# Kernel tuning notes

Hardware: AMD Instinct MI355X
Metric: run time of the kernel (lower is better)

The kernel has to match this reference:

```python
import jax, jax.numpy as jnp
import numpy as np

jax.config.update("jax_enable_x64", True)  # needed for faithful int64 topology hash (31**i weights)

B, SEQ, HID, OUT = 64, 2048, 1024, 1024
MAX_DEPTH = 3
MAX_NODES = 2 ** MAX_DEPTH - 1          # 7
MAX_LEAVES = 2 ** (MAX_DEPTH - 1)       # 4 leaf slots (nodes 3..6)
MAX_SHAPE_IDS = 256


def _gelu(x):
    return jax.nn.gelu(x, approximate=False)  # torch nn.GELU default = exact erf


def setup_inputs() -> dict:
    key = jax.random.key(0)
    ks = jax.random.split(key, 8)
    states = jax.random.normal(ks[0], (B, SEQ, HID), dtype=jnp.float32)

    rng = np.random.default_rng(0)
    lengths = rng.integers(SEQ // 2, SEQ, size=(B,)).astype(np.int64)
    # sorted segment boundaries within [0, lengths), first boundary at 0
    fr = np.sort(rng.random((B, MAX_LEAVES - 1)), axis=1)
    boundaries = np.concatenate(
        [np.zeros((B, 1), np.int64), np.floor(fr * lengths[:, None]).astype(np.int64)], axis=1)
    mask = np.arange(SEQ)[None, :] < lengths[:, None]
    # complete binary tree, depth 3: node 0 root, nodes 1-2 internal, 3-6 leaves
    leaf_order = np.tile(np.arange(MAX_NODES // 2, MAX_NODES, dtype=np.int64), (B, 1))
    active = np.ones((B, MAX_NODES), bool)
    is_leaf = np.concatenate([np.zeros((B, 3), bool), np.ones((B, 4), bool)], axis=1)
    left_child = np.array([1, 3, 5, -1, -1, -1, -1], np.int64)
    right_child = np.array([2, 4, 6, -1, -1, -1, -1], np.int64)
    depth = np.array([0, 1, 1, 2, 2, 2, 2], np.int64)

    def lin(k, fan_in, shape):
        return jax.random.normal(k, shape, dtype=jnp.float32) / np.sqrt(fan_in).astype(np.float32)

    W1 = lin(ks[1], HID, (HID, OUT)); b1 = jnp.zeros((OUT,), jnp.float32)
    W2 = lin(ks[2], OUT, (OUT, OUT)); b2 = jnp.zeros((OUT,), jnp.float32)
    Wm1 = lin(ks[3], 2 * OUT, (2 * OUT, OUT)); bm1 = jnp.zeros((OUT,), jnp.float32)
    Wm2 = lin(ks[4], OUT, (OUT, OUT)); bm2 = jnp.zeros((OUT,), jnp.float32)
    depth_embed = jax.random.normal(ks[5], (MAX_DEPTH, OUT), dtype=jnp.float32) * 0.02
    shape_embed = jax.random.normal(ks[6], (MAX_SHAPE_IDS, OUT), dtype=jnp.float32) * 0.02

    return dict(
        states=states, mask=jnp.asarray(mask), lengths=jnp.asarray(lengths),
        boundaries=jnp.asarray(boundaries), leaf_order=jnp.asarray(leaf_order),
        active=jnp.asarray(active), is_leaf=jnp.asarray(is_leaf),
        left_child=jnp.asarray(left_child), right_child=jnp.asarray(right_child),
        depth=jnp.asarray(depth),
        W1=W1, b1=b1, W2=W2, b2=b2, Wm1=Wm1, bm1=bm1, Wm2=Wm2, bm2=bm2,
        depth_embed=depth_embed, shape_embed=shape_embed)


def _forward(states, W1, b1, W2, b2, Wm1, bm1, Wm2, bm2, depth_embed, shape_embed,
             mask, lengths, boundaries, leaf_order, active, is_leaf,
             left_child, right_child, depth):
    b, seq, _ = states.shape
    S = boundaries.shape[1]
    max_nodes = left_child.shape[0]

    # ---- 1. vectorized ragged masked segment-mean pooling ----
    pos = jnp.arange(seq)
    # segment id per token: number of boundaries <= t, minus 1
    seg_id = (pos[None, None, :] >= boundaries[:, :, None]).sum(1) - 1      # (b, seq)
    valid = mask & (pos[None, :] < lengths[:, None]) & (seg_id >= 0)
    onehot = ((seg_id[:, :, None] == jnp.arange(S)[None, None, :])
              & valid[:, :, None]).astype(states.dtype)                     # (b, seq, S)
    cnt = onehot.sum(1)                                                     # (b, S)
    pooled = jnp.einsum('bts,bth->bsh', onehot, states) / jnp.clip(cnt, 1.0)[..., None]

    # ---- 2. encode segments + depth embedding, scatter to leaf slots ----
    enc = _gelu(pooled @ W1 + b1) @ W2 + b2                                 # (b, S, D)
    nidx = leaf_order                                                       # (b, S)
    nclip = jnp.maximum(nidx, 0)
    enc = enc + depth_embed[depth[nclip]]
    leaf_ok = (nidx >= 0) & jnp.take_along_axis(is_leaf, nclip, axis=1) & (cnt > 0)
    contrib = enc * leaf_ok[..., None].astype(enc.dtype)
    node_repr = jnp.zeros((b, max_nodes, enc.shape[-1]), enc.dtype)
    node_repr = node_repr.at[jnp.arange(b)[:, None], nclip].add(contrib)

    # ---- 3. bottom-up binary tree merge (loop over fixed small node count) ----
    for i in range(max_nodes - 1, -1, -1):
        lc = left_child[i]
        rc = right_child[i]
        is_int = active[:, i] & ~is_leaf[:, i]                              # (b,)
        l = jnp.take(node_repr, jnp.maximum(lc, 0), axis=1)                 # (b, D)
        r = jnp.take(node_repr, jnp.maximum(rc, 0), axis=1)
        merged = (_gelu(jnp.concatenate([l, r], axis=-1) @ Wm1 + bm1) @ Wm2 + bm2
                  + depth_embed[depth[i]])
        upd = is_int.any() & (lc != -1)
        newv = jnp.where(upd, merged * is_int[:, None].astype(merged.dtype),
                         node_repr[:, i])
        node_repr = node_repr.at[:, i].set(newv)

    # ---- 4. topology hash -> shape embedding ----
    pattern = active.astype(jnp.int64) * 2 + is_leaf.astype(jnp.int64)      # (b, nodes)
    weights = 31 ** jnp.arange(max_nodes, dtype=jnp.int64)
    hashed = (pattern * weights[None, :]).sum(1)
    shape_ids = jnp.abs(hashed) % shape_embed.shape[0]
    return node_repr[:, 0] + shape_embed[shape_ids]


def reference(states, mask, lengths, boundaries, leaf_order, active, is_leaf,
              left_child, right_child, depth,
              W1, b1, W2, b2, Wm1, bm1, Wm2, bm2, depth_embed, shape_embed):
    return _forward(states, W1, b1, W2, b2, Wm1, bm1, Wm2, bm2,
                    depth_embed, shape_embed, mask, lengths, boundaries,
                    leaf_order, active, is_leaf, left_child, right_child, depth)
```

## Files before the change

kernel.cpp:

```cpp
#include <hip/hip_runtime.h>
#include <cstdint>
#include <cstddef>

#define SEQ   2048
#define HID   1024
#define NBAT  64
#define NSEG  4
#define NNODE 7
#define TCHUNK 128

__device__ __forceinline__ float gelu_f(float x) {
  return 0.5f * x * (1.0f + erff(x * 0.7071067811865476f));
}

__global__ __launch_bounds__(256) void pool_kernel(
    const float* __restrict__ states, const int* __restrict__ boundaries,
    const int* __restrict__ lengths, float* __restrict__ pooled_sum)
{
  const int tc = blockIdx.x, b = blockIdx.y;
  const int tid = threadIdx.x;
  const int len = lengths[b];
  int bnd[5];
  bnd[0] = boundaries[b * 4 + 0];
  bnd[1] = boundaries[b * 4 + 1];
  bnd[2] = boundaries[b * 4 + 2];
  bnd[3] = boundaries[b * 4 + 3];
  bnd[4] = len;
  const int clo = tc * TCHUNK, chi = clo + TCHUNK;
  const float4* S = (const float4*)(states + (size_t)b * SEQ * HID);

  #pragma unroll
  for (int s = 0; s < NSEG; ++s) {
    int lo = bnd[s]     > clo ? bnd[s]     : clo;
    int hi = bnd[s + 1] < chi ? bnd[s + 1] : chi;
    if (lo >= hi) continue;
    float4 acc = make_float4(0.f, 0.f, 0.f, 0.f);
    int t = lo;
    for (; t + 4 <= hi; t += 4) {
      float4 v0 = S[(size_t)(t + 0) * (HID / 4) + tid];
      float4 v1 = S[(size_t)(t + 1) * (HID / 4) + tid];
      float4 v2 = S[(size_t)(t + 2) * (HID / 4) + tid];
      float4 v3 = S[(size_t)(t + 3) * (HID / 4) + tid];
      acc.x += (v0.x + v1.x) + (v2.x + v3.x);
      acc.y += (v0.y + v1.y) + (v2.y + v3.y);
      acc.z += (v0.z + v1.z) + (v2.z + v3.z);
      acc.w += (v0.w + v1.w) + (v2.w + v3.w);
    }
    for (; t < hi; ++t) {
      float4 v = S[(size_t)t * (HID / 4) + tid];
      acc.x += v.x; acc.y += v.y; acc.z += v.z; acc.w += v.w;
    }
    float* dst = pooled_sum + (size_t)(b * NSEG + s) * HID + tid * 4;
    atomicAdd(dst + 0, acc.x);
    atomicAdd(dst + 1, acc.y);
    atomicAdd(dst + 2, acc.z);
    atomicAdd(dst + 3, acc.w);
  }
}

#define BM 32
#define BN 64
#define BK 32

template<int AMODE, int EPI>
__global__ __launch_bounds__(256) void gemm_kernel(
    const float* __restrict__ A, const float* __restrict__ W,
    const float* __restrict__ bias, float* __restrict__ C,
    int M, int K,
    const int* __restrict__ boundaries, const int* __restrict__ lengths,
    const int* __restrict__ leaf_order, const int* __restrict__ active,
    const int* __restrict__ is_leaf, const int* __restrict__ depth,
    const int* __restrict__ left_child, const int* __restrict__ right_child,
    const float* __restrict__ dembed, const float* __restrict__ sembed,
    const float* __restrict__ node_in, float* __restrict__ node_out,
    int nodeA, int nodeB)
{
  const int N = 1024;
  __shared__ float As[BK][BM + 2];
  __shared__ float Ws[BK][BN];

  const int tid = threadIdx.x;
  const int n0 = blockIdx.x * BN;
  const int m0 = blockIdx.y * BM;

  const int am = tid >> 3;
  const int ak = (tid & 7) * 4;
  const int wk = tid >> 3;
  const int wn = (tid & 7) * 8;
  const int rm = (tid >> 4) * 2;
  const int cn = (tid & 15) * 4;

  float ainv = 1.0f;
  int lcn = 0, rcn = 0, arow_b = 0;
  if (AMODE == 1) {
    int m = m0 + am; int b = m >> 2; int s = m & 3;
    int bs = boundaries[b * 4 + s];
    int bn = (s < 3) ? boundaries[b * 4 + s + 1] : lengths[b];
    ainv = 1.0f / fmaxf((float)(bn - bs), 1.0f);
  } else if (AMODE == 2) {
    int mrow = m0 + am; int mi = mrow >> 6; int b = mrow & 63;
    int node = mi ? nodeB : nodeA;
    lcn = left_child[node]; rcn = right_child[node];
    arow_b = b;
  }

  float acc[2][4] = {{0.f,0.f,0.f,0.f},{0.f,0.f,0.f,0.f}};

  float4 av, wv0, wv1;
  {
    if (AMODE == 2) {
      int col = ak;
      int child = (col < 1024) ? lcn : rcn;
      av = *(const float4*)(node_in + (size_t)(arow_b * NNODE + child) * 1024 + (col & 1023));
    } else {
      av = *(const float4*)(A + (size_t)(m0 + am) * K + ak);
    }
    wv0 = *(const float4*)(W + (size_t)wk * N + n0 + wn);
    wv1 = *(const float4*)(W + (size_t)wk * N + n0 + wn + 4);
  }

  for (int k0 = 0; k0 < K; k0 += BK) {
    __syncthreads();
    As[ak + 0][am] = av.x * ainv;
    As[ak + 1][am] = av.y * ainv;
    As[ak + 2][am] = av.z * ainv;
    As[ak + 3][am] = av.w * ainv;
    *(float4*)&Ws[wk][wn]     = wv0;
    *(float4*)&Ws[wk][wn + 4] = wv1;
    __syncthreads();

    const int kn = k0 + BK;
    if (kn < K) {
      if (AMODE == 2) {
        int col = kn + ak;
        int child = (col < 1024) ? lcn : rcn;
        av = *(const float4*)(node_in + (size_t)(arow_b * NNODE + child) * 1024 + (col & 1023));
      } else {
        av = *(const float4*)(A + (size_t)(m0 + am) * K + kn + ak);
      }
      wv0 = *(const float4*)(W + (size_t)(kn + wk) * N + n0 + wn);
      wv1 = *(const float4*)(W + (size_t)(kn + wk) * N + n0 + wn + 4);
    }

    #pragma unroll
    for (int kk = 0; kk < BK; ++kk) {
      float2 a2 = *(const float2*)&As[kk][rm];
      float4 w  = *(const float4*)&Ws[kk][cn];
      acc[0][0] += a2.x * w.x; acc[0][1] += a2.x * w.y;
      acc[0][2] += a2.x * w.z; acc[0][3] += a2.x * w.w;
      acc[1][0] += a2.y * w.x; acc[1][1] += a2.y * w.y;
      acc[1][2] += a2.y * w.z; acc[1][3] += a2.y * w.w;
    }
  }

  #pragma unroll
  for (int r = 0; r < 2; ++r) {
    const int m = m0 + rm + r;
    const int n = n0 + cn;
    float4 x;
    x.x = acc[r][0] + bias[n + 0];
    x.y = acc[r][1] + bias[n + 1];
    x.z = acc[r][2] + bias[n + 2];
    x.w = acc[r][3] + bias[n + 3];

    if (EPI == 0) {
      x.x = gelu_f(x.x); x.y = gelu_f(x.y); x.z = gelu_f(x.z); x.w = gelu_f(x.w);
      *(float4*)(C + (size_t)m * N + n) = x;
    } else if (EPI == 1) {
      int b = m >> 2; int s = m & 3;
      int node  = leaf_order[b * 4 + s];
      int nclip = node < 0 ? 0 : node;
      int bs = boundaries[b * 4 + s];
      int bn = (s < 3) ? boundaries[b * 4 + s + 1] : lengths[b];
      bool ok = (node >= 0) && (is_leaf[b * NNODE + nclip] != 0) && (bn - bs > 0);
      int d = depth[nclip];
      const float* de = dembed + (size_t)d * 1024 + n;
      float sc = ok ? 1.0f : 0.0f;
      x.x = (x.x + de[0]) * sc; x.y = (x.y + de[1]) * sc;
      x.z = (x.z + de[2]) * sc; x.w = (x.w + de[3]) * sc;
      *(float4*)(node_out + (size_t)(b * NNODE + nclip) * 1024 + n) = x;
    } else if (EPI == 2) {
      int mi = m >> 6; int b = m & 63;
      int node = mi ? nodeB : nodeA;
      bool ii = (active[b * NNODE + node] != 0) && (is_leaf[b * NNODE + node] == 0);
      int d = depth[node];
      const float* de = dembed + (size_t)d * 1024 + n;
      float sc = ii ? 1.0f : 0.0f;
      x.x = (x.x + de[0]) * sc; x.y = (x.y + de[1]) * sc;
      x.z = (x.z + de[2]) * sc; x.w = (x.w + de[3]) * sc;
      *(float4*)(node_out + (size_t)(b * NNODE + node) * 1024 + n) = x;
    } else {
      int b = m & 63;
      bool ii = (active[b * NNODE + 0] != 0) && (is_leaf[b * NNODE + 0] == 0);
      int d = depth[0];
      const float* de = dembed + (size_t)d * 1024 + n;
      float sc = ii ? 1.0f : 0.0f;
      long long h = 0, w = 1;
      #pragma unroll
      for (int i = 0; i < NNODE; ++i) {
        long long p = (long long)active[b * NNODE + i] * 2
                    + (long long)is_leaf[b * NNODE + i];
        h += p * w;
        w *= 31;
      }
      long long a = h < 0 ? -h : h;
      int sid = (int)(a % 256);
      const float* se = sembed + (size_t)sid * 1024 + n;
      x.x = (x.x + de[0]) * sc + se[0];
      x.y = (x.y + de[1]) * sc + se[1];
      x.z = (x.z + de[2]) * sc + se[2];
      x.w = (x.w + de[3]) * sc + se[3];
      *(float4*)(node_out + (size_t)b * 1024 + n) = x;
    }
  }
}

extern "C" void kernel_launch(void* const* d_in, const int* in_sizes, int n_in,
                              void* d_out, int out_size, void* d_ws, size_t ws_size,
                              hipStream_t stream)
{
  const float* states     = (const float*)d_in[0];
  const int* lengths      = (const int*)d_in[2];
  const int* boundaries   = (const int*)d_in[3];
  const int* leaf_order   = (const int*)d_in[4];
  const int* active       = (const int*)d_in[5];
  const int* is_leaf      = (const int*)d_in[6];
  const int* left_child   = (const int*)d_in[7];
  const int* right_child  = (const int*)d_in[8];
  const int* depth        = (const int*)d_in[9];
  const float* W1  = (const float*)d_in[10];
  const float* b1  = (const float*)d_in[11];
  const float* W2  = (const float*)d_in[12];
  const float* b2  = (const float*)d_in[13];
  const float* Wm1 = (const float*)d_in[14];
  const float* bm1 = (const float*)d_in[15];
  const float* Wm2 = (const float*)d_in[16];
  const float* bm2 = (const float*)d_in[17];
  const float* dembed = (const float*)d_in[18];
  const float* sembed = (const float*)d_in[19];
  float* out = (float*)d_out;

  float* pooled    = (float*)d_ws;
  float* H1        = pooled + 256 * 1024;
  float* Hm        = H1 + 256 * 1024;
  float* node_repr = Hm + 128 * 1024;

  hipMemsetAsync(pooled, 0, (size_t)256 * 1024 * sizeof(float), stream);

  pool_kernel<<<dim3(SEQ / TCHUNK, NBAT), 256, 0, stream>>>(
      states, boundaries, lengths, pooled);

  gemm_kernel<1, 0><<<dim3(16, 8), 256, 0, stream>>>(
      pooled, W1, b1, H1, 256, 1024,
      boundaries, lengths, leaf_order, active, is_leaf, depth,
      left_child, right_child, dembed, sembed, nullptr, nullptr, -1, -1);

  gemm_kernel<0, 1><<<dim3(16, 8), 256, 0, stream>>>(
      H1, W2, b2, nullptr, 256, 1024,
      boundaries, lengths, leaf_order, active, is_leaf, depth,
      left_child, right_child, dembed, sembed, nullptr, node_repr, -1, -1);

  gemm_kernel<2, 0><<<dim3(16, 4), 256, 0, stream>>>(
      nullptr, Wm1, bm1, Hm, 128, 2048,
      boundaries, lengths, leaf_order, active, is_leaf, depth,
      left_child, right_child, dembed, sembed, node_repr, nullptr, 1, 2);
  gemm_kernel<0, 2><<<dim3(16, 4), 256, 0, stream>>>(
      Hm, Wm2, bm2, nullptr, 128, 1024,
      boundaries, lengths, leaf_order, active, is_leaf, depth,
      left_child, right_child, dembed, sembed, nullptr, node_repr, 1, 2);

  gemm_kernel<2, 0><<<dim3(16, 2), 256, 0, stream>>>(
      nullptr, Wm1, bm1, Hm, 64, 2048,
      boundaries, lengths, leaf_order, active, is_leaf, depth,
      left_child, right_child, dembed, sembed, node_repr, nullptr, 0, 0);
  gemm_kernel<0, 3><<<dim3(16, 2), 256, 0, stream>>>(
      Hm, Wm2, bm2, nullptr, 64, 1024,
      boundaries, lengths, leaf_order, active, is_leaf, depth,
      left_child, right_child, dembed, sembed, nullptr, out, 0, 0);
}
```

Baseline: 966.7 us.

## Split-K the tree GEMMs and fuse partial reduction with bias-GELU into A-loads

Each GEMM now splits K across blockIdx.z and writes partial sums to workspace. The following GEMM sums the partials, adds bias and applies GELU while loading its A tile. Separate small reduction kernels apply the bias and node epilogues. This raises block counts for the small-M tree GEMMs, which previously launched only 32-128 blocks, at the cost of extra partial-buffer traffic, redundant GELU recompute, and more launches.

New measurement: 812.2 us. 16.0% less time.

```diff
diff --git a/kernel.cpp b/kernel.cpp
--- a/kernel.cpp
+++ b/kernel.cpp
@@ -62,18 +62,16 @@
 #define BN 64
 #define BK 32
 
-template<int AMODE, int EPI>
+template<int AMODE, int SPLIT, int SRCS>
 __global__ __launch_bounds__(256) void gemm_kernel(
-    const float* __restrict__ A, const float* __restrict__ W,
-    const float* __restrict__ bias, float* __restrict__ C,
+    const float* __restrict__ A,
+    const float* __restrict__ W,
+    const float* __restrict__ biasA,
+    float* __restrict__ Cp,
     int M, int K,
     const int* __restrict__ boundaries, const int* __restrict__ lengths,
-    const int* __restrict__ leaf_order, const int* __restrict__ active,
-    const int* __restrict__ is_leaf, const int* __restrict__ depth,
     const int* __restrict__ left_child, const int* __restrict__ right_child,
-    const float* __restrict__ dembed, const float* __restrict__ sembed,
-    const float* __restrict__ node_in, float* __restrict__ node_out,
-    int nodeA, int nodeB)
+    const float* __restrict__ node_in, int nodeA, int nodeB)
 {
   const int N = 1024;
   __shared__ float As[BK][BM + 2];
@@ -82,6 +80,9 @@
   const int tid = threadIdx.x;
   const int n0 = blockIdx.x * BN;
   const int m0 = blockIdx.y * BM;
+  const int z  = blockIdx.z;
+  const int Kloc = K / SPLIT;
+  const int kbeg = z * Kloc;
 
   const int am = tid >> 3;
   const int ak = (tid & 7) * 4;
@@ -92,12 +93,12 @@
 
   float ainv = 1.0f;
   int lcn = 0, rcn = 0, arow_b = 0;
-  if (AMODE == 1) {
+  if constexpr (AMODE == 1) {
     int m = m0 + am; int b = m >> 2; int s = m & 3;
     int bs = boundaries[b * 4 + s];
     int bn = (s < 3) ? boundaries[b * 4 + s + 1] : lengths[b];
     ainv = 1.0f / fmaxf((float)(bn - bs), 1.0f);
-  } else if (AMODE == 2) {
+  } else if constexpr (AMODE == 2) {
     int mrow = m0 + am; int mi = mrow >> 6; int b = mrow & 63;
     int node = mi ? nodeB : nodeA;
     lcn = left_child[node]; rcn = right_child[node];
@@ -106,40 +107,58 @@
 
   float acc[2][4] = {{0.f,0.f,0.f,0.f},{0.f,0.f,0.f,0.f}};
 
-  float4 av, wv0, wv1;
-  {
-    if (AMODE == 2) {
-      int col = ak;
-      int child = (col < 1024) ? lcn : rcn;
-      av = *(const float4*)(node_in + (size_t)(arow_b * NNODE + child) * 1024 + (col & 1023));
+  float4 av[SRCS]; float4 bv; float4 wv0, wv1;
+
+  auto issueA = [&](int kcol) {
+    if constexpr (AMODE == 3) {
+      #pragma unroll
+      for (int s = 0; s < SRCS; ++s)
+        av[s] = *(const float4*)(A + ((size_t)s * M + (m0 + am)) * (size_t)K + kcol);
+      bv = *(const float4*)(biasA + kcol);
+    } else if constexpr (AMODE == 2) {
+      int child = (kcol < 1024) ? lcn : rcn;
+      av[0] = *(const float4*)(node_in + (size_t)(arow_b * NNODE + child) * 1024 + (kcol & 1023));
     } else {
-      av = *(const float4*)(A + (size_t)(m0 + am) * K + ak);
-    }
-    wv0 = *(const float4*)(W + (size_t)wk * N + n0 + wn);
-    wv1 = *(const float4*)(W + (size_t)wk * N + n0 + wn + 4);
-  }
-
-  for (int k0 = 0; k0 < K; k0 += BK) {
+      av[0] = *(const float4*)(A + (size_t)(m0 + am) * K + kcol);
+    }
+  };
+
+  issueA(kbeg + ak);
+  wv0 = *(const float4*)(W + (size_t)(kbeg + wk) * N + n0 + wn);
+  wv1 = *(const float4*)(W + (size_t)(kbeg + wk) * N + n0 + wn + 4);
+
+  for (int k0 = 0; k0 < Kloc; k0 += BK) {
     __syncthreads();
-    As[ak + 0][am] = av.x * ainv;
-    As[ak + 1][am] = av.y * ainv;
-    As[ak + 2][am] = av.z * ainv;
-    As[ak + 3][am] = av.w * ainv;
+    {
+      float4 a;
+      if constexpr (AMODE == 3) {
+        float4 s = av[0];
+        #pragma unroll
+        for (int q = 1; q < SRCS; ++q) {
+          s.x += av[q].x; s.y += av[q].y; s.z += av[q].z; s.w += av[q].w;
+        }
+        a.x = gelu_f(s.x + bv.x); a.y = gelu_f(s.y + bv.y);
+        a.z = gelu_f(s.z + bv.z); a.w = gelu_f(s.w + bv.w);
+      } else if constexpr (AMODE == 1) {
+        a = av[0];
+        a.x *= ainv; a.y *= ainv; a.z *= ainv; a.w *= ainv;
+      } else {
+        a = av[0];
+      }
+      As[ak + 0][am] = a.x;
+      As[ak + 1][am] = a.y;
+      As[ak + 2][am] = a.z;
+      As[ak + 3][am] = a.w;
+    }
     *(float4*)&Ws[wk][wn]     = wv0;
     *(float4*)&Ws[wk][wn + 4] = wv1;
     __syncthreads();
 
     const int kn = k0 + BK;
-    if (kn < K) {
-      if (AMODE == 2) {
-        int col = kn + ak;
-        int child = (col < 1024) ? lcn : rcn;
-        av = *(const float4*)(node_in + (size_t)(arow_b * NNODE + child) * 1024 + (col & 1023));
-      } else {
-        av = *(const float4*)(A + (size_t)(m0 + am) * K + kn + ak);
-      }
-      wv0 = *(const float4*)(W + (size_t)(kn + wk) * N + n0 + wn);
-      wv1 = *(const float4*)(W + (size_t)(kn + wk) * N + n0 + wn + 4);
+    if (kn < Kloc) {
+      issueA(kbeg + kn + ak);
+      wv0 = *(const float4*)(W + (size_t)(kbeg + kn + wk) * N + n0 + wn);
+      wv1 = *(const float4*)(W + (size_t)(kbeg + kn + wk) * N + n0 + wn + 4);
     }
 
     #pragma unroll
@@ -156,62 +175,77 @@
   #pragma unroll
   for (int r = 0; r < 2; ++r) {
     const int m = m0 + rm + r;
-    const int n = n0 + cn;
-    float4 x;
-    x.x = acc[r][0] + bias[n + 0];
-    x.y = acc[r][1] + bias[n + 1];
-    x.z = acc[r][2] + bias[n + 2];
-    x.w = acc[r][3] + bias[n + 3];
-
-    if (EPI == 0) {
-      x.x = gelu_f(x.x); x.y = gelu_f(x.y); x.z = gelu_f(x.z); x.w = gelu_f(x.w);
-      *(float4*)(C + (size_t)m * N + n) = x;
-    } else if (EPI == 1) {
-      int b = m >> 2; int s = m & 3;
-      int node  = leaf_order[b * 4 + s];
-      int nclip = node < 0 ? 0 : node;
-      int bs = boundaries[b * 4 + s];
-      int bn = (s < 3) ? boundaries[b * 4 + s + 1] : lengths[b];
-      bool ok = (node >= 0) && (is_leaf[b * NNODE + nclip] != 0) && (bn - bs > 0);
-      int d = depth[nclip];
-      const float* de = dembed + (size_t)d * 1024 + n;
-      float sc = ok ? 1.0f : 0.0f;
-      x.x = (x.x + de[0]) * sc; x.y = (x.y + de[1]) * sc;
-      x.z = (x.z + de[2]) * sc; x.w = (x.w + de[3]) * sc;
-      *(float4*)(node_out + (size_t)(b * NNODE + nclip) * 1024 + n) = x;
-    } else if (EPI == 2) {
-      int mi = m >> 6; int b = m & 63;
-      int node = mi ? nodeB : nodeA;
-      bool ii = (active[b * NNODE + node] != 0) && (is_leaf[b * NNODE + node] == 0);
-      int d = depth[node];
-      const float* de = dembed + (size_t)d * 1024 + n;
-      float sc = ii ? 1.0f : 0.0f;
-      x.x = (x.x + de[0]) * sc; x.y = (x.y + de[1]) * sc;
-      x.z = (x.z + de[2]) * sc; x.w = (x.w + de[3]) * sc;
-      *(float4*)(node_out + (size_t)(b * NNODE + node) * 1024 + n) = x;
-    } else {
-      int b = m & 63;
-      bool ii = (active[b * NNODE + 0] != 0) && (is_leaf[b * NNODE + 0] == 0);
-      int d = depth[0];
-      const float* de = dembed + (size_t)d * 1024 + n;
-      float sc = ii ? 1.0f : 0.0f;
-      long long h = 0, w = 1;
-      #pragma unroll
-      for (int i = 0; i < NNODE; ++i) {
-        long long p = (long long)active[b * NNODE + i] * 2
-                    + (long long)is_leaf[b * NNODE + i];
-        h += p * w;
-        w *= 31;
-      }
-      long long a = h < 0 ? -h : h;
-      int sid = (int)(a % 256);
-      const float* se = sembed + (size_t)sid * 1024 + n;
-      x.x = (x.x + de[0]) * sc + se[0];
-      x.y = (x.y + de[1]) * sc + se[1];
-      x.z = (x.z + de[2]) * sc + se[2];
-      x.w = (x.w + de[3]) * sc + se[3];
-      *(float4*)(node_out + (size_t)b * 1024 + n) = x;
-    }
+    *(float4*)(Cp + ((size_t)z * M + m) * N + n0 + cn) =
+        make_float4(acc[r][0], acc[r][1], acc[r][2], acc[r][3]);
+  }
+}
+
+template<int EPI, int SRCS>
+__global__ __launch_bounds__(256) void redepi_kernel(
+    const float* __restrict__ P, const float* __restrict__ bias, int M,
+    const int* __restrict__ boundaries, const int* __restrict__ lengths,
+    const int* __restrict__ leaf_order, const int* __restrict__ active,
+    const int* __restrict__ is_leaf, const int* __restrict__ depth,
+    const float* __restrict__ dembed, const float* __restrict__ sembed,
+    float* __restrict__ node_out, int nodeA, int nodeB)
+{
+  const int m = blockIdx.x;
+  const int n = threadIdx.x * 4;
+
+  float4 x = *(const float4*)(P + (size_t)m * 1024 + n);
+  #pragma unroll
+  for (int q = 1; q < SRCS; ++q) {
+    float4 p = *(const float4*)(P + ((size_t)q * M + m) * 1024 + n);
+    x.x += p.x; x.y += p.y; x.z += p.z; x.w += p.w;
+  }
+  x.x += bias[n + 0]; x.y += bias[n + 1];
+  x.z += bias[n + 2]; x.w += bias[n + 3];
+
+  if constexpr (EPI == 1) {
+    int b = m >> 2; int s = m & 3;
+    int node  = leaf_order[b * 4 + s];
+    int nclip = node < 0 ? 0 : node;
+    int bs = boundaries[b * 4 + s];
+    int bn = (s < 3) ? boundaries[b * 4 + s + 1] : lengths[b];
+    bool ok = (node >= 0) && (is_leaf[b * NNODE + nclip] != 0) && (bn - bs > 0);
+    int d = depth[nclip];
+    const float* de = dembed + (size_t)d * 1024 + n;
+    float sc = ok ? 1.0f : 0.0f;
+    x.x = (x.x + de[0]) * sc; x.y = (x.y + de[1]) * sc;
+    x.z = (x.z + de[2]) * sc; x.w = (x.w + de[3]) * sc;
+    *(float4*)(node_out + (size_t)(b * NNODE + nclip) * 1024 + n) = x;
+  } else if constexpr (EPI == 2) {
+    int mi = m >> 6; int b = m & 63;
+    int node = mi ? nodeB : nodeA;
+    bool ii = (active[b * NNODE + node] != 0) && (is_leaf[b * NNODE + node] == 0);
+    int d = depth[node];
+    const float* de = dembed + (size_t)d * 1024 + n;
+    float sc = ii ? 1.0f : 0.0f;
+    x.x = (x.x + de[0]) * sc; x.y = (x.y + de[1]) * sc;
+    x.z = (x.z + de[2]) * sc; x.w = (x.w + de[3]) * sc;
+    *(float4*)(node_out + (size_t)(b * NNODE + node) * 1024 + n) = x;
+  } else {
+    int b = m & 63;
+    bool ii = (active[b * NNODE + 0] != 0) && (is_leaf[b * NNODE + 0] == 0);
+    int d = depth[0];
+    const float* de = dembed + (size_t)d * 1024 + n;
+    float sc = ii ? 1.0f : 0.0f;
+    long long h = 0, w = 1;
+    #pragma unroll
+    for (int i = 0; i < NNODE; ++i) {
+      long long p = (long long)active[b * NNODE + i] * 2
+                  + (long long)is_leaf[b * NNODE + i];
+      h += p * w;
+      w *= 31;
+    }
+    long long a = h < 0 ? -h : h;
+    int sid = (int)(a % 256);
+    const float* se = sembed + (size_t)sid * 1024 + n;
+    x.x = (x.x + de[0]) * sc + se[0];
+    x.y = (x.y + de[1]) * sc + se[1];
+    x.z = (x.z + de[2]) * sc + se[2];
+    x.w = (x.w + de[3]) * sc + se[3];
+    *(float4*)(node_out + (size_t)b * 1024 + n) = x;
   }
 }
 
@@ -241,40 +275,52 @@
   float* out = (float*)d_out;
 
   float* pooled    = (float*)d_ws;
-  float* H1        = pooled + 256 * 1024;
-  float* Hm        = H1 + 256 * 1024;
-  float* node_repr = Hm + 128 * 1024;
+  float* P1 = pooled + 256 * 1024;
+  float* P2 = P1 + 2 * 256 * 1024;
+  float* P3 = P2 + 2 * 256 * 1024;
+  float* P4 = P3 + 4 * 128 * 1024;
+  float* P5 = P4 + 4 * 128 * 1024;
+  float* P6 = P5 + 8 * 64 * 1024;
+  float* node_repr = P6 + 8 * 64 * 1024;
 
   hipMemsetAsync(pooled, 0, (size_t)256 * 1024 * sizeof(float), stream);
 
   pool_kernel<<<dim3(SEQ / TCHUNK, NBAT), 256, 0, stream>>>(
       states, boundaries, lengths, pooled);
 
-  gemm_kernel<1, 0><<<dim3(16, 8), 256, 0, stream>>>(
-      pooled, W1, b1, H1, 256, 1024,
-      boundaries, lengths, leaf_order, active, is_leaf, depth,
-      left_child, right_child, dembed, sembed, nullptr, nullptr, -1, -1);
-
-  gemm_kernel<0, 1><<<dim3(16, 8), 256, 0, stream>>>(
-      H1, W2, b2, nullptr, 256, 1024,
-      boundaries, lengths, leaf_order, active, is_leaf, depth,
-      left_child, right_child, dembed, sembed, nullptr, node_repr, -1, -1);
-
-  gemm_kernel<2, 0><<<dim3(16, 4), 256, 0, stream>>>(
-      nullptr, Wm1, bm1, Hm, 128, 2048,
-      boundaries, lengths, leaf_order, active, is_leaf, depth,
-      left_child, right_child, dembed, sembed, node_repr, nullptr, 1, 2);
-  gemm_kernel<0, 2><<<dim3(16, 4), 256, 0, stream>>>(
-      Hm, Wm2, bm2, nullptr, 128, 1024,
-      boundaries, lengths, leaf_order, active, is_leaf, depth,
-      left_child, right_child, dembed, sembed, nullptr, node_repr, 1, 2);
-
-  gemm_kernel<2, 0><<<dim3(16, 2), 256, 0, stream>>>(
-      nullptr, Wm1, bm1, Hm, 64, 2048,
-      boundaries, lengths, leaf_order, active, is_leaf, depth,
-      left_child, right_child, dembed, sembed, node_repr, nullptr, 0, 0);
-  gemm_kernel<0, 3><<<dim3(16, 2), 256, 0, stream>>>(
-      Hm, Wm2, bm2, nullptr, 64, 1024,
-      boundaries, lengths, leaf_order, active, is_leaf, depth,
-      left_child, right_child, dembed, sembed, nullptr, out, 0, 0);
-}
+  gemm_kernel<1, 2, 1><<<dim3(16, 8, 2), 256, 0, stream>>>(
+      pooled, W1, nullptr, P1, 256, 1024,
+      boundaries, lengths, nullptr, nullptr, nullptr, -1, -1);
+
+  gemm_kernel<3, 2, 2><<<dim3(16, 8, 2), 256, 0, stream>>>(
+      P1, W2, b1, P2, 256, 1024,
+      nullptr, nullptr, nullptr, nullptr, nullptr, -1, -1);
+
+  redepi_kernel<1, 2><<<dim3(256), 256, 0, stream>>>(
+      P2, b2, 256, boundaries, lengths, leaf_order, active, is_leaf, depth,
+      dembed, sembed, node_repr, -1, -1);
+
+  gemm_kernel<2, 4, 1><<<dim3(16, 4, 4), 256, 0, stream>>>(
+      nullptr, Wm1, nullptr, P3, 128, 2048,
+      nullptr, nullptr, left_child, right_child, node_repr, 1, 2);
+
+  gemm_kernel<3, 4, 4><<<dim3(16, 4, 4), 256, 0, stream>>>(
+      P3, Wm2, bm1, P4, 128, 1024,
+      nullptr, nullptr, nullptr, nullptr, nullptr, -1, -1);
+
+  redepi_kernel<2, 4><<<dim3(128), 256, 0, stream>>>(
+      P4, bm2, 128, boundaries, lengths, leaf_order, active, is_leaf, depth,
+      dembed, sembed, node_repr, 1, 2);
+
+  gemm_kernel<2, 8, 1><<<dim3(16, 2, 8), 256, 0, stream>>>(
+      nullptr, Wm1, nullptr, P5, 64, 2048,
+      nullptr, nullptr, left_child, right_child, node_repr, 0, 0);
+
+  gemm_kernel<3, 8, 8><<<dim3(16, 2, 8), 256, 0, stream>>>(
+      P5, Wm2, bm1, P6, 64, 1024,
+      nullptr, nullptr, nullptr, nullptr, nullptr, -1, -1);
+
+  redepi_kernel<3, 8><<<dim3(64), 256, 0, stream>>>(
+      P6, bm2, 64, boundaries, lengths, leaf_order, active, is_leaf, depth,
+      dembed, sembed, out, 0, 0);
+}
```
